# Kernel tuning notes

Measured on AMD Instinct MI355X. Metric: run time of the kernel, lower is better.

Reference implementation:

```python
import jax, jax.numpy as jnp
import numpy as np

NEG_SLOPE = 0.2  # PyG GATv2Conv default

N_NODES = 10000
N_EDGES = 320000
DIM_IN = 128
DIM_H = 32
HEADS = 8
DIM_OUT = 32
HID = DIM_H * HEADS  # 256


def _gatv2(x, src, dst, Wl, Wr, att, bias, heads, ch, n):
    # x: [N, Fin]; src/dst: [E] (self-loops already included)
    xl = (x @ Wl).reshape(n, heads, ch)  # source-side transform
    xr = (x @ Wr).reshape(n, heads, ch)  # target-side transform
    e = jax.nn.leaky_relu(xl[src] + xr[dst], NEG_SLOPE)       # [E, H, C]
    score = jnp.einsum('ehc,hc->eh', e, att)                  # [E, H]
    m = jax.ops.segment_max(score, dst, num_segments=n)        # [N, H]
    ex = jnp.exp(score - m[dst])
    denom = jax.ops.segment_sum(ex, dst, num_segments=n)
    alpha = ex / (denom[dst] + 1e-16)                          # [E, H]
    out = jax.ops.segment_sum(alpha[:, :, None] * xl[src], dst, num_segments=n)
    return out.reshape(n, heads * ch) + bias


def setup_inputs() -> dict:
    key = jax.random.key(0)
    ks = jax.random.split(key, 16)
    x = jax.random.normal(ks[0], (N_NODES, DIM_IN), dtype=jnp.float32)
    edge_index = jax.random.randint(ks[1], (2, N_EDGES), 0, N_NODES, dtype=jnp.int64)

    def glorot(k, shape, fan_in):
        return jax.random.normal(k, shape, dtype=jnp.float32) * (1.0 / np.sqrt(fan_in))

    return {
        'x': x,
        'W1l': glorot(ks[2], (DIM_IN, HID), DIM_IN),
        'W1r': glorot(ks[3], (DIM_IN, HID), DIM_IN),
        'a1': glorot(ks[4], (HEADS, DIM_H), DIM_H),
        'b1': jnp.zeros((HID,), dtype=jnp.float32),
        'W2l': glorot(ks[5], (HID, HID), HID),
        'W2r': glorot(ks[6], (HID, HID), HID),
        'a2': glorot(ks[7], (HEADS, DIM_H), DIM_H),
        'b2': jnp.zeros((HID,), dtype=jnp.float32),
        'W3l': glorot(ks[8], (HID, DIM_OUT), HID),
        'W3r': glorot(ks[9], (HID, DIM_OUT), HID),
        'a3': glorot(ks[10], (1, DIM_OUT), DIM_OUT),
        'b3': jnp.zeros((DIM_OUT,), dtype=jnp.float32),
        'edge_index': edge_index,
    }


def reference(x, W1l, W1r, a1, b1, W2l, W2r, a2, b2, W3l, W3r, a3, b3, edge_index):
    n = x.shape[0]
    loops = jnp.arange(n, dtype=edge_index.dtype)
    src = jnp.concatenate([edge_index[0], loops])
    dst = jnp.concatenate([edge_index[1], loops])

    # eval mode: dropout(p=0.6) is identity
    h = _gatv2(x, src, dst, W1l, W1r, a1, b1, HEADS, DIM_H, n)
    h = jax.nn.relu(h)
    h_res = h
    h = _gatv2(h, src, dst, W2l, W2r, a2, b2, HEADS, DIM_H, n)
    h = h + h_res
    h = _gatv2(h, src, dst, W3l, W3r, a3, b3, 1, DIM_OUT, n)
    return h
```

## Files before the change

kernel.cpp:

```cpp
#include <hip/hip_runtime.h>

#define N_NODES 10000
#define N_EDGES 320000
#define E_TOT   (N_EDGES + N_NODES)
#define HID 256
#define NEG_SLOPE 0.2f
#define SLOTS 192

typedef __attribute__((ext_vector_type(8))) short short8;
typedef __attribute__((ext_vector_type(4))) float float4v;

__device__ int   g_cnt[N_NODES];
__device__ int   g_csr[(size_t)N_NODES * SLOTS];
__device__ __align__(16) float g_xl[(size_t)N_NODES * HID];
__device__ __align__(16) float g_xr[(size_t)N_NODES * HID];
__device__ __align__(16) float g_h1[(size_t)N_NODES * HID];
__device__ __align__(16) unsigned short g_xlb[(size_t)N_NODES * HID];
__device__ __align__(16) unsigned short g_abf[(size_t)N_NODES * 512];
__device__ __align__(16) unsigned short g_bp1a[16 * 8  * 64 * 8];
__device__ __align__(16) unsigned short g_bp2a[16 * 8  * 64 * 8];
__device__ __align__(16) unsigned short g_bp1b[16 * 16 * 64 * 8];
__device__ __align__(16) unsigned short g_bp2b[16 * 16 * 64 * 8];
__device__ __align__(16) unsigned short g_bp1c[2  * 16 * 64 * 8];
__device__ __align__(16) unsigned short g_bp2c[2  * 16 * 64 * 8];

#define LOG2E 1.44269504088896340736f

__device__ __forceinline__ unsigned short f2bf(float f) {
    unsigned int u = __float_as_uint(f);
    unsigned int r = (u + 0x7fffu + ((u >> 16) & 1u)) >> 16;
    return (unsigned short)r;
}
__device__ __forceinline__ float bf2f(unsigned short h) {
    return __uint_as_float(((unsigned int)h) << 16);
}
__device__ __forceinline__ unsigned int splitpack(float f) {
    unsigned short hi = f2bf(f);
    unsigned short lo = f2bf(f - bf2f(hi));
    return ((unsigned int)lo << 16) | hi;
}

__device__ __forceinline__ void packB(const float* __restrict__ B,
                                      unsigned short* __restrict__ Bp,
                                      int t, int nkc, int N) {
    int lane = t & 63;
    int kc   = (t >> 6) % nkc;
    int nt   = (t >> 6) / nkc;
    int n = nt * 16 + (lane & 15);
    int kbase = kc * 32 + (lane >> 4) * 8;
    #pragma unroll
    for (int j = 0; j < 8; ++j) {
        int kp = kbase + j;
        int k  = kp >> 1;
        float f = B[(size_t)k * N + n];
        unsigned short hi = f2bf(f);
        Bp[(size_t)t * 8 + j] = (kp & 1) ? f2bf(f - bf2f(hi)) : hi;
    }
}

__global__ __launch_bounds__(256) void k_prep(const float* __restrict__ W1l,
                                              const float* __restrict__ W1r,
                                              const float* __restrict__ W2l,
                                              const float* __restrict__ W2r,
                                              const float* __restrict__ W3l,
                                              const float* __restrict__ W3r,
                                              int* __restrict__ cnt) {
    const int S0 = 16 * 8 * 64;
    const int S1 = 16 * 16 * 64;
    const int S2 = 2 * 16 * 64;
    int t = blockIdx.x * blockDim.x + threadIdx.x;
    if (t < S0) {
        packB(W1l, g_bp1a, t, 8, 256);
        packB(W1r, g_bp2a, t, 8, 256);
    } else if (t < S0 + S1) {
        int u = t - S0;
        packB(W2l, g_bp1b, u, 16, 256);
        packB(W2r, g_bp2b, u, 16, 256);
    } else if (t < S0 + S1 + S2) {
        int u = t - S0 - S1;
        packB(W3l, g_bp1c, u, 16, 32);
        packB(W3r, g_bp2c, u, 16, 32);
    } else {
        int u = t - S0 - S1 - S2;
        if (u < N_NODES) cnt[u] = 0;
    }
}

#define FILL_BLOCKS ((E_TOT + 255) / 256)
__global__ __launch_bounds__(256) void k_fill_gemm1(
    const int* __restrict__ ei,
    int* __restrict__ cnt, int* __restrict__ csr,
    const float4* __restrict__ A4,
    const short8* __restrict__ Bp1, const short8* __restrict__ Bp2,
    unsigned short* __restrict__ C1b,
    float* __restrict__ C2)
{
    if (blockIdx.x < FILL_BLOCKS) {
        int e = blockIdx.x * 256 + threadIdx.x;
        if (e < E_TOT) {
            int src, dst;
            if (e < N_EDGES) { src = ei[e]; dst = ei[N_EDGES + e]; }
            else             { src = dst = e - N_EDGES; }
            int pos = atomicAdd(&cnt[dst], 1);
            if (pos < SLOTS) csr[dst * SLOTS + pos] = src;
        }
        return;
    }
    const int nkc = 8;
    int mt   = blockIdx.x - FILL_BLOCKS;
    int lane = threadIdx.x & 63;
    int wid  = threadIdx.x >> 6;
    int quad = lane >> 4;
    int col  = lane & 15;
    int r0 = mt * 32 + col;       if (r0 >= N_NODES) r0 = N_NODES - 1;
    int r1 = mt * 32 + 16 + col;  if (r1 >= N_NODES) r1 = N_NODES - 1;
    const float4* a0 = A4 + (size_t)r0 * 32 + quad;
    const float4* a1 = A4 + (size_t)r1 * 32 + quad;
    float4v acc[2][4][2];
    #pragma unroll
    for (int s = 0; s < 2; ++s)
        #pragma unroll
        for (int t = 0; t < 4; ++t) { acc[s][t][0] = (float4v)(0.f); acc[s][t][1] = (float4v)(0.f); }
    for (int kc = 0; kc < nkc; ++kc) {
        float4 v0 = a0[kc * 4];
        float4 v1 = a1[kc * 4];
        union { short8 s; unsigned int u[4]; } c0, c1;
        c0.u[0] = splitpack(v0.x); c0.u[1] = splitpack(v0.y);
        c0.u[2] = splitpack(v0.z); c0.u[3] = splitpack(v0.w);
        c1.u[0] = splitpack(v1.x); c1.u[1] = splitpack(v1.y);
        c1.u[2] = splitpack(v1.z); c1.u[3] = splitpack(v1.w);
        short8 A0 = c0.s, A1 = c1.s;
        #pragma unroll
        for (int t = 0; t < 4; ++t) {
            int nt = wid * 4 + t;
            size_t bi = ((size_t)(nt * nkc + kc)) * 64 + lane;
            short8 b1 = Bp1[bi];
            short8 b2 = Bp2[bi];
            acc[0][t][0] = __builtin_amdgcn_mfma_f32_16x16x32_bf16(A0, b1, acc[0][t][0], 0, 0, 0);
            acc[0][t][1] = __builtin_amdgcn_mfma_f32_16x16x32_bf16(A0, b2, acc[0][t][1], 0, 0, 0);
            acc[1][t][0] = __builtin_amdgcn_mfma_f32_16x16x32_bf16(A1, b1, acc[1][t][0], 0, 0, 0);
            acc[1][t][1] = __builtin_amdgcn_mfma_f32_16x16x32_bf16(A1, b2, acc[1][t][1], 0, 0, 0);
        }
    }
    #pragma unroll
    for (int s = 0; s < 2; ++s) {
        #pragma unroll
        for (int t = 0; t < 4; ++t) {
            int gc = (wid * 4 + t) * 16 + col;
            #pragma unroll
            for (int r = 0; r < 4; ++r) {
                int row = mt * 32 + s * 16 + quad * 4 + r;
                if (row < N_NODES) {
                    C1b[(size_t)row * 256 + gc] = f2bf(acc[s][t][0][r]);
                    C2[(size_t)row * 256 + gc]  = acc[s][t][1][r];
                }
            }
        }
    }
}

__global__ __launch_bounds__(256) void k_mgemm2(const short8* __restrict__ Af,
                                                const short8* __restrict__ Bp1,
                                                const short8* __restrict__ Bp2,
                                                unsigned short* __restrict__ C1b,
                                                float* __restrict__ C2,
                                                int Kp, int nkc) {
    int mt   = blockIdx.x;
    int lane = threadIdx.x & 63;
    int wid  = threadIdx.x >> 6;
    int quad = lane >> 4;
    int col  = lane & 15;
    int ks   = Kp >> 3;
    int r0 = mt * 32 + col;       if (r0 >= N_NODES) r0 = N_NODES - 1;
    int r1 = mt * 32 + 16 + col;  if (r1 >= N_NODES) r1 = N_NODES - 1;
    const short8* a0 = Af + (size_t)r0 * ks + quad;
    const short8* a1 = Af + (size_t)r1 * ks + quad;
    float4v acc[2][4][2];
    #pragma unroll
    for (int s = 0; s < 2; ++s)
        #pragma unroll
        for (int t = 0; t < 4; ++t) { acc[s][t][0] = (float4v)(0.f); acc[s][t][1] = (float4v)(0.f); }
    for (int kc = 0; kc < nkc; ++kc) {
        short8 A0 = a0[kc * 4];
        short8 A1 = a1[kc * 4];
        #pragma unroll
        for (int t = 0; t < 4; ++t) {
            int nt = wid * 4 + t;
            size_t bi = ((size_t)(nt * nkc + kc)) * 64 + lane;
            short8 b1 = Bp1[bi];
            short8 b2 = Bp2[bi];
            acc[0][t][0] = __builtin_amdgcn_mfma_f32_16x16x32_bf16(A0, b1, acc[0][t][0], 0, 0, 0);
            acc[0][t][1] = __builtin_amdgcn_mfma_f32_16x16x32_bf16(A0, b2, acc[0][t][1], 0, 0, 0);
            acc[1][t][0] = __builtin_amdgcn_mfma_f32_16x16x32_bf16(A1, b1, acc[1][t][0], 0, 0, 0);
            acc[1][t][1] = __builtin_amdgcn_mfma_f32_16x16x32_bf16(A1, b2, acc[1][t][1], 0, 0, 0);
        }
    }
    #pragma unroll
    for (int s = 0; s < 2; ++s) {
        #pragma unroll
        for (int t = 0; t < 4; ++t) {
            int gc = (wid * 4 + t) * 16 + col;
            #pragma unroll
            for (int r = 0; r < 4; ++r) {
                int row = mt * 32 + s * 16 + quad * 4 + r;
                if (row < N_NODES) {
                    C1b[(size_t)row * 256 + gc] = f2bf(acc[s][t][0][r]);
                    C2[(size_t)row * 256 + gc]  = acc[s][t][1][r];
                }
            }
        }
    }
}

__global__ __launch_bounds__(256) void k_mgemm32(const short8* __restrict__ Af,
                                                 const short8* __restrict__ Bp1,
                                                 const short8* __restrict__ Bp2,
                                                 float* __restrict__ C1,
                                                 float* __restrict__ C2) {
    int mt   = blockIdx.x;
    int lane = threadIdx.x & 63;
    int wid  = threadIdx.x >> 6;
    int quad = lane >> 4;
    int col  = lane & 15;
    int nt   = wid & 1;
    const short8* Bp = (wid < 2) ? Bp1 : Bp2;
    float* C = (wid < 2) ? C1 : C2;

    const short8* abase = Af + (size_t)(mt * 16 + col) * 64 + quad;
    float4v acc = (float4v)(0.f);
    #pragma unroll 4
    for (int kc = 0; kc < 16; ++kc) {
        short8 a = abase[kc * 4];
        short8 b = Bp[((size_t)(nt * 16 + kc)) * 64 + lane];
        acc = __builtin_amdgcn_mfma_f32_16x16x32_bf16(a, b, acc, 0, 0, 0);
    }
    #pragma unroll
    for (int r = 0; r < 4; ++r)
        C[(size_t)(mt * 16 + quad * 4 + r) * 32 + nt * 16 + col] = acc[r];
}

__global__ __launch_bounds__(256) void k_agg8(const unsigned short* __restrict__ xlb,
                                              const float4* __restrict__ xr4,
                                              const float4* __restrict__ att4,
                                              const float4* __restrict__ bias4,
                                              const int* __restrict__ cnt,
                                              const int* __restrict__ csr_src,
                                              const float4* __restrict__ res4,
                                              float4* __restrict__ out4,
                                              uint4* __restrict__ abf_out,
                                              int mode) {
    __shared__ float  ss[4][64];
    __shared__ float4 sacc[4][64];
    int node = blockIdx.x;
    int lane = threadIdx.x & 63;
    int wid  = threadIdx.x >> 6;
    float4 xrv = xr4[(size_t)node * 64 + lane];
    float4 av  = att4[lane];
    av.x *= LOG2E; av.y *= LOG2E; av.z *= LOG2E; av.w *= LOG2E;
    int c = cnt[node]; if (c > SLOTS) c = SLOTS;
    int start = node * SLOTS, end = start + c;
    int span = (c + 3) >> 2;
    int wbeg = start + wid * span;
    int wend = wbeg + span; if (wend > end) wend = end;
    int nloc = wend - wbeg;

    int ldi = wbeg + lane;
    int idxv = csr_src[ldi < end ? ldi : (end - 1)];

    float s = 0.f;
    float4 acc = make_float4(0.f, 0.f, 0.f, 0.f);

    for (int j0 = 0; j0 < nloc; j0 += 4) {
        int srcs[4];
        ushort4 uv[4];
        #pragma unroll
        for (int j = 0; j < 4; ++j)
            srcs[j] = __shfl(idxv, j0 + j);
        #pragma unroll
        for (int j = 0; j < 4; ++j)
            uv[j] = *(const ushort4*)(xlb + (size_t)srcs[j] * 256 + 4 * lane);
        #pragma unroll
        for (int j = 0; j < 4; ++j) {
            if (j0 + j < nloc) {
                float4 xv;
                xv.x = bf2f(uv[j].x); xv.y = bf2f(uv[j].y);
                xv.z = bf2f(uv[j].z); xv.w = bf2f(uv[j].w);
                float tx = xv.x + xrv.x, ty = xv.y + xrv.y;
                float tz = xv.z + xrv.z, tw = xv.w + xrv.w;
                float w = fmaxf(tx, NEG_SLOPE * tx) * av.x
                        + fmaxf(ty, NEG_SLOPE * ty) * av.y
                        + fmaxf(tz, NEG_SLOPE * tz) * av.z
                        + fmaxf(tw, NEG_SLOPE * tw) * av.w;
                w += __shfl_xor(w, 1);
                w += __shfl_xor(w, 2);
                w += __shfl_xor(w, 4);
                float p = exp2f(w);
                s += p;
                acc.x += p * xv.x;
                acc.y += p * xv.y;
                acc.z += p * xv.z;
                acc.w += p * xv.w;
            }
        }
    }
    ss[wid][lane] = s;
    sacc[wid][lane] = acc;
    __syncthreads();
    if (wid == 0) {
        float S = ss[0][lane] + ss[1][lane] + ss[2][lane] + ss[3][lane];
        float4 A = make_float4(0.f, 0.f, 0.f, 0.f);
        #pragma unroll
        for (int w = 0; w < 4; ++w) {
            float4 a = sacc[w][lane];
            A.x += a.x; A.y += a.y; A.z += a.z; A.w += a.w;
        }
        float inv = 1.f / (S + 1e-16f);
        float4 bv = bias4[lane];
        float4 o;
        o.x = A.x * inv + bv.x; o.y = A.y * inv + bv.y;
        o.z = A.z * inv + bv.z; o.w = A.w * inv + bv.w;
        if (mode == 0) {
            o.x = fmaxf(o.x, 0.f); o.y = fmaxf(o.y, 0.f);
            o.z = fmaxf(o.z, 0.f); o.w = fmaxf(o.w, 0.f);
        } else {
            float4 r = res4[(size_t)node * 64 + lane];
            o.x += r.x; o.y += r.y; o.z += r.z; o.w += r.w;
        }
        if (out4) out4[(size_t)node * 64 + lane] = o;
        if (abf_out) {
            uint4 u;
            u.x = splitpack(o.x); u.y = splitpack(o.y);
            u.z = splitpack(o.z); u.w = splitpack(o.w);
            abf_out[(size_t)node * 64 + lane] = u;
        }
    }
}

__global__ __launch_bounds__(256) void k_agg1(const float4* __restrict__ xl4,
                                              const float4* __restrict__ xr4,
                                              const float4* __restrict__ att4,
                                              const float4* __restrict__ bias4,
                                              const int* __restrict__ cnt,
                                              const int* __restrict__ csr_src,
                                              float4* __restrict__ out4) {
    int node = blockIdx.x * 4 + (threadIdx.x >> 6);
    if (node >= N_NODES) return;
    int lane = threadIdx.x & 63;
    int q = lane & 7;
    int grp = lane >> 3;
    float4 xrv = xr4[(size_t)node * 8 + q];
    float4 av  = att4[q];
    av.x *= LOG2E; av.y *= LOG2E; av.z *= LOG2E; av.w *= LOG2E;
    int c = cnt[node]; if (c > SLOTS) c = SLOTS;
    int start = node * SLOTS, end = start + c;
    float s = 0.f;
    float4 acc = make_float4(0.f, 0.f, 0.f, 0.f);
    for (int i = start + grp; i < end; i += 8) {
        int src = csr_src[i];
        float4 xv = xl4[(size_t)src * 8 + q];
        float tx = xv.x + xrv.x, ty = xv.y + xrv.y;
        float tz = xv.z + xrv.z, tw = xv.w + xrv.w;
        float w = fmaxf(tx, NEG_SLOPE * tx) * av.x
                + fmaxf(ty, NEG_SLOPE * ty) * av.y
                + fmaxf(tz, NEG_SLOPE * tz) * av.z
                + fmaxf(tw, NEG_SLOPE * tw) * av.w;
        w += __shfl_xor(w, 1);
        w += __shfl_xor(w, 2);
        w += __shfl_xor(w, 4);
        float p = exp2f(w);
        s += p;
        acc.x += p * xv.x;
        acc.y += p * xv.y;
        acc.z += p * xv.z;
        acc.w += p * xv.w;
    }
    #pragma unroll
    for (int off = 8; off < 64; off <<= 1) {
        s     += __shfl_xor(s, off);
        acc.x += __shfl_xor(acc.x, off);
        acc.y += __shfl_xor(acc.y, off);
        acc.z += __shfl_xor(acc.z, off);
        acc.w += __shfl_xor(acc.w, off);
    }
    if (grp == 0) {
        float inv = 1.f / (s + 1e-16f);
        float4 bv = bias4[q];
        float4 o;
        o.x = acc.x * inv + bv.x; o.y = acc.y * inv + bv.y;
        o.z = acc.z * inv + bv.z; o.w = acc.w * inv + bv.w;
        out4[(size_t)node * 8 + q] = o;
    }
}


extern "C" void kernel_launch(void* const* d_in, const int* in_sizes, int n_in,
                              void* d_out, int out_size, void* d_ws, size_t ws_size,
                              hipStream_t stream) {
    const float* x   = (const float*)d_in[0];
    const float* W1l = (const float*)d_in[1];
    const float* W1r = (const float*)d_in[2];
    const float* a1  = (const float*)d_in[3];
    const float* b1  = (const float*)d_in[4];
    const float* W2l = (const float*)d_in[5];
    const float* W2r = (const float*)d_in[6];
    const float* a2  = (const float*)d_in[7];
    const float* b2  = (const float*)d_in[8];
    const float* W3l = (const float*)d_in[9];
    const float* W3r = (const float*)d_in[10];
    const float* a3  = (const float*)d_in[11];
    const float* b3  = (const float*)d_in[12];
    const int*   ei  = (const int*)d_in[13];
    float* out = (float*)d_out;

    int *cnt, *csr;
    float *xl, *xr, *h1;
    unsigned short *xlb, *abf, *bp1a, *bp2a, *bp1b, *bp2b, *bp1c, *bp2c;
    hipGetSymbolAddress((void**)&cnt,    HIP_SYMBOL(g_cnt));
    hipGetSymbolAddress((void**)&csr,    HIP_SYMBOL(g_csr));
    hipGetSymbolAddress((void**)&xl,     HIP_SYMBOL(g_xl));
    hipGetSymbolAddress((void**)&xr,     HIP_SYMBOL(g_xr));
    hipGetSymbolAddress((void**)&h1,     HIP_SYMBOL(g_h1));
    hipGetSymbolAddress((void**)&xlb,    HIP_SYMBOL(g_xlb));
    hipGetSymbolAddress((void**)&abf,    HIP_SYMBOL(g_abf));
    hipGetSymbolAddress((void**)&bp1a,   HIP_SYMBOL(g_bp1a));
    hipGetSymbolAddress((void**)&bp2a,   HIP_SYMBOL(g_bp2a));
    hipGetSymbolAddress((void**)&bp1b,   HIP_SYMBOL(g_bp1b));
    hipGetSymbolAddress((void**)&bp2b,   HIP_SYMBOL(g_bp2b));
    hipGetSymbolAddress((void**)&bp1c,   HIP_SYMBOL(g_bp1c));
    hipGetSymbolAddress((void**)&bp2c,   HIP_SYMBOL(g_bp2c));

    k_prep<<<144, 256, 0, stream>>>(W1l, W1r, W2l, W2r, W3l, W3r, cnt);

    k_fill_gemm1<<<FILL_BLOCKS + (N_NODES + 31) / 32, 256, 0, stream>>>(
        ei, cnt, csr, (const float4*)x,
        (const short8*)bp1a, (const short8*)bp2a, xlb, xr);

    k_agg8<<<N_NODES, 256, 0, stream>>>(xlb, (const float4*)xr,
                                        (const float4*)a1, (const float4*)b1,
                                        cnt, csr, nullptr, (float4*)h1,
                                        (uint4*)abf, 0);

    k_mgemm2<<<(N_NODES + 31) / 32, 256, 0, stream>>>((const short8*)abf,
                                                      (const short8*)bp1b, (const short8*)bp2b,
                                                      xlb, xr, 512, 16);

    k_agg8<<<N_NODES, 256, 0, stream>>>(xlb, (const float4*)xr,
                                        (const float4*)a2, (const float4*)b2,
                                        cnt, csr, (const float4*)h1, nullptr,
                                        (uint4*)abf, 1);

    k_mgemm32<<<N_NODES / 16, 256, 0, stream>>>((const short8*)abf,
                                                (const short8*)bp1c, (const short8*)bp2c,
                                                xl, xr);

    k_agg1<<<(N_NODES + 3) / 4, 256, 0, stream>>>((const float4*)xl, (const float4*)xr,
                                                  (const float4*)a3, (const float4*)b3,
                                                  cnt, csr, (float4*)out);
}
```

Before: 222.5 us.

## Fold weight packing into fill kernel and reset edge counters in final aggregation

Removes the separate prep kernel launch. The layer-2 and layer-3 weight packing moves into extra blocks of the fill/GEMM1 kernel. GEMM1 now converts W1l/W1r from fp32 into split-bf16 operands inline instead of reading prepacked buffers. Zeroing of the per-node edge counters moves to the end of the last aggregation kernel, so it relies on counters starting at zero from static initialization and from the previous call. The aim is one fewer launch and dependency; the cost is redundant, less coalesced W1 loads and conversion work in every GEMM1 block.

```diff
diff --git a/kernel.cpp b/kernel.cpp
--- a/kernel.cpp
+++ b/kernel.cpp
@@ -17,8 +17,6 @@
 __device__ __align__(16) float g_h1[(size_t)N_NODES * HID];
 __device__ __align__(16) unsigned short g_xlb[(size_t)N_NODES * HID];
 __device__ __align__(16) unsigned short g_abf[(size_t)N_NODES * 512];
-__device__ __align__(16) unsigned short g_bp1a[16 * 8  * 64 * 8];
-__device__ __align__(16) unsigned short g_bp2a[16 * 8  * 64 * 8];
 __device__ __align__(16) unsigned short g_bp1b[16 * 16 * 64 * 8];
 __device__ __align__(16) unsigned short g_bp2b[16 * 16 * 64 * 8];
 __device__ __align__(16) unsigned short g_bp1c[2  * 16 * 64 * 8];
@@ -58,40 +56,18 @@
     }
 }
 
-__global__ __launch_bounds__(256) void k_prep(const float* __restrict__ W1l,
-                                              const float* __restrict__ W1r,
-                                              const float* __restrict__ W2l,
-                                              const float* __restrict__ W2r,
-                                              const float* __restrict__ W3l,
-                                              const float* __restrict__ W3r,
-                                              int* __restrict__ cnt) {
-    const int S0 = 16 * 8 * 64;
-    const int S1 = 16 * 16 * 64;
-    const int S2 = 2 * 16 * 64;
-    int t = blockIdx.x * blockDim.x + threadIdx.x;
-    if (t < S0) {
-        packB(W1l, g_bp1a, t, 8, 256);
-        packB(W1r, g_bp2a, t, 8, 256);
-    } else if (t < S0 + S1) {
-        int u = t - S0;
-        packB(W2l, g_bp1b, u, 16, 256);
-        packB(W2r, g_bp2b, u, 16, 256);
-    } else if (t < S0 + S1 + S2) {
-        int u = t - S0 - S1;
-        packB(W3l, g_bp1c, u, 16, 32);
-        packB(W3r, g_bp2c, u, 16, 32);
-    } else {
-        int u = t - S0 - S1 - S2;
-        if (u < N_NODES) cnt[u] = 0;
-    }
-}
-
 #define FILL_BLOCKS ((E_TOT + 255) / 256)
-__global__ __launch_bounds__(256) void k_fill_gemm1(
+#define GEMM1_TILES ((N_NODES + 31) / 32)
+#define MEGA_G1     (FILL_BLOCKS + GEMM1_TILES)
+#define MEGA_PB     (MEGA_G1 + 64)
+#define MEGA_PC     (MEGA_PB + 8)
+__global__ __launch_bounds__(256) void k_mega(
     const int* __restrict__ ei,
     int* __restrict__ cnt, int* __restrict__ csr,
     const float4* __restrict__ A4,
-    const short8* __restrict__ Bp1, const short8* __restrict__ Bp2,
+    const float* __restrict__ W1l, const float* __restrict__ W1r,
+    const float* __restrict__ W2l, const float* __restrict__ W2r,
+    const float* __restrict__ W3l, const float* __restrict__ W3r,
     unsigned short* __restrict__ C1b,
     float* __restrict__ C2)
 {
@@ -106,12 +82,26 @@
         }
         return;
     }
+    if (blockIdx.x >= MEGA_G1) {
+        if (blockIdx.x < MEGA_PB) {
+            int u = (blockIdx.x - MEGA_G1) * 256 + threadIdx.x;
+            packB(W2l, g_bp1b, u, 16, 256);
+            packB(W2r, g_bp2b, u, 16, 256);
+        } else if (blockIdx.x < MEGA_PC) {
+            int u = (blockIdx.x - MEGA_PB) * 256 + threadIdx.x;
+            packB(W3l, g_bp1c, u, 16, 32);
+            packB(W3r, g_bp2c, u, 16, 32);
+        }
+        return;
+    }
     const int nkc = 8;
     int mt   = blockIdx.x - FILL_BLOCKS;
     int lane = threadIdx.x & 63;
     int wid  = threadIdx.x >> 6;
     int quad = lane >> 4;
     int col  = lane & 15;
+    int bn = lane & 15;
+    int bk = (lane >> 4) * 4;
     int r0 = mt * 32 + col;       if (r0 >= N_NODES) r0 = N_NODES - 1;
     int r1 = mt * 32 + 16 + col;  if (r1 >= N_NODES) r1 = N_NODES - 1;
     const float4* a0 = A4 + (size_t)r0 * 32 + quad;
@@ -130,12 +120,19 @@
         c1.u[0] = splitpack(v1.x); c1.u[1] = splitpack(v1.y);
         c1.u[2] = splitpack(v1.z); c1.u[3] = splitpack(v1.w);
         short8 A0 = c0.s, A1 = c1.s;
+        int k0 = kc * 16 + bk;
         #pragma unroll
         for (int t = 0; t < 4; ++t) {
-            int nt = wid * 4 + t;
-            size_t bi = ((size_t)(nt * nkc + kc)) * 64 + lane;
-            short8 b1 = Bp1[bi];
-            short8 b2 = Bp2[bi];
+            int n = (wid * 4 + t) * 16 + bn;
+            const float* w1p = W1l + (size_t)k0 * 256 + n;
+            const float* w2p = W1r + (size_t)k0 * 256 + n;
+            union { short8 s; unsigned int u[4]; } b1v, b2v;
+            #pragma unroll
+            for (int m = 0; m < 4; ++m) {
+                b1v.u[m] = splitpack(w1p[(size_t)m * 256]);
+                b2v.u[m] = splitpack(w2p[(size_t)m * 256]);
+            }
+            short8 b1 = b1v.s, b2 = b2v.s;
             acc[0][t][0] = __builtin_amdgcn_mfma_f32_16x16x32_bf16(A0, b1, acc[0][t][0], 0, 0, 0);
             acc[0][t][1] = __builtin_amdgcn_mfma_f32_16x16x32_bf16(A0, b2, acc[0][t][1], 0, 0, 0);
             acc[1][t][0] = __builtin_amdgcn_mfma_f32_16x16x32_bf16(A1, b1, acc[1][t][0], 0, 0, 0);
@@ -340,7 +337,7 @@
                                               const float4* __restrict__ xr4,
                                               const float4* __restrict__ att4,
                                               const float4* __restrict__ bias4,
-                                              const int* __restrict__ cnt,
+                                              int* __restrict__ cnt,
                                               const int* __restrict__ csr_src,
                                               float4* __restrict__ out4) {
     int node = blockIdx.x * 4 + (threadIdx.x >> 6);
@@ -389,6 +386,7 @@
         o.x = acc.x * inv + bv.x; o.y = acc.y * inv + bv.y;
         o.z = acc.z * inv + bv.z; o.w = acc.w * inv + bv.w;
         out4[(size_t)node * 8 + q] = o;
+        if (q == 0) cnt[node] = 0;
     }
 }
 
@@ -414,7 +412,7 @@
 
     int *cnt, *csr;
     float *xl, *xr, *h1;
-    unsigned short *xlb, *abf, *bp1a, *bp2a, *bp1b, *bp2b, *bp1c, *bp2c;
+    unsigned short *xlb, *abf, *bp1b, *bp2b, *bp1c, *bp2c;
     hipGetSymbolAddress((void**)&cnt,    HIP_SYMBOL(g_cnt));
     hipGetSymbolAddress((void**)&csr,    HIP_SYMBOL(g_csr));
     hipGetSymbolAddress((void**)&xl,     HIP_SYMBOL(g_xl));
@@ -422,18 +420,14 @@
     hipGetSymbolAddress((void**)&h1,     HIP_SYMBOL(g_h1));
     hipGetSymbolAddress((void**)&xlb,    HIP_SYMBOL(g_xlb));
     hipGetSymbolAddress((void**)&abf,    HIP_SYMBOL(g_abf));
-    hipGetSymbolAddress((void**)&bp1a,   HIP_SYMBOL(g_bp1a));
-    hipGetSymbolAddress((void**)&bp2a,   HIP_SYMBOL(g_bp2a));
     hipGetSymbolAddress((void**)&bp1b,   HIP_SYMBOL(g_bp1b));
     hipGetSymbolAddress((void**)&bp2b,   HIP_SYMBOL(g_bp2b));
     hipGetSymbolAddress((void**)&bp1c,   HIP_SYMBOL(g_bp1c));
     hipGetSymbolAddress((void**)&bp2c,   HIP_SYMBOL(g_bp2c));
 
-    k_prep<<<144, 256, 0, stream>>>(W1l, W1r, W2l, W2r, W3l, W3r, cnt);
-
-    k_fill_gemm1<<<FILL_BLOCKS + (N_NODES + 31) / 32, 256, 0, stream>>>(
-        ei, cnt, csr, (const float4*)x,
-        (const short8*)bp1a, (const short8*)bp2a, xlb, xr);
+    k_mega<<<MEGA_PC, 256, 0, stream>>>(ei, cnt, csr, (const float4*)x,
+                                        W1l, W1r, W2l, W2r, W3l, W3r,
+                                        xlb, xr);
 
     k_agg8<<<N_NODES, 256, 0, stream>>>(xlb, (const float4*)xr,
                                         (const float4*)a1, (const float4*)b1,
```

After: 234.5 us. 1.05x slower.
